# Optimization experiments

Measured on AMD Instinct MI355X. Metric: run time of the kernel, lower is better.

## Reference

```python
import jax, jax.numpy as jnp
import numpy as np

H = 16        # heads
DH = 64       # dim_head
DM = 1024     # query_dim = context_dim
INNER = H * DH


def setup_inputs() -> dict:
    key = jax.random.key(0)
    ks = jax.random.split(key, 5)
    s = 0.02
    queries = jax.random.normal(ks[0], (2, 2048, DM), dtype=jnp.float32)
    Wq = jax.random.normal(ks[1], (DM, INNER), dtype=jnp.float32) * s
    Wkv = jax.random.normal(ks[2], (DM, 2 * INNER), dtype=jnp.float32) * s
    Wo = jax.random.normal(ks[3], (INNER, DM), dtype=jnp.float32) * s
    bo = jax.random.normal(ks[4], (DM,), dtype=jnp.float32) * s
    return {"queries": queries, "Wq": Wq, "Wkv": Wkv, "Wo": Wo, "bo": bo}


def reference(queries, Wq, Wkv, Wo, bo):
    b, n, _ = queries.shape
    scale = DH ** -0.5
    q = queries @ Wq                       # [b, n, inner]
    kv = queries @ Wkv                     # self-attention: context = queries
    k, v = jnp.split(kv, 2, axis=-1)
    # b n (h d) -> b h n d
    split_heads = lambda t: t.reshape(b, n, H, DH).transpose(0, 2, 1, 3)
    q, k, v = map(split_heads, (q, k, v))
    sim = jnp.einsum('bhid,bhjd->bhij', q, k) * scale
    attn = jax.nn.softmax(sim, axis=-1)    # dropout is identity (p=0 / eval)
    out = jnp.einsum('bhij,bhjd->bhid', attn, v)
    out = out.transpose(0, 2, 1, 3).reshape(b, n, INNER)
    return out @ Wo + bo
```

## Files before the change

### kernel.cpp

```cpp
#include <hip/hip_runtime.h>
#include <math.h>
#include <stdint.h>

typedef _Float16 half8v __attribute__((ext_vector_type(8)));
typedef _Float16 half4v __attribute__((ext_vector_type(4)));
typedef float floatx4 __attribute__((ext_vector_type(4)));

#define MFMA16(a, b, c) __builtin_amdgcn_mfma_f32_16x16x32_f16(a, b, c, 0, 0, 0)

#define QSCALE 0.18033688011112f

__device__ __forceinline__ void gld_lds16(const void* g, void* l) {
  __builtin_amdgcn_global_load_lds(
      (const __attribute__((address_space(1))) uint32_t*)(uintptr_t)g,
      (__attribute__((address_space(3))) uint32_t*)(uintptr_t)l, 16, 0, 0);
}

__global__ __launch_bounds__(256) void convert_x(
    const float* __restrict__ X, _Float16* __restrict__ X16)
{
  size_t gid = (size_t)blockIdx.x * 256 + threadIdx.x;
  const float4* src = (const float4*)(X) + gid * 2;
  float4 a = src[0], b = src[1];
  half8v h;
  h[0]=(_Float16)a.x; h[1]=(_Float16)a.y; h[2]=(_Float16)a.z; h[3]=(_Float16)a.w;
  h[4]=(_Float16)b.x; h[5]=(_Float16)b.y; h[6]=(_Float16)b.z; h[7]=(_Float16)b.w;
  *((half8v*)X16 + gid) = h;
}

__global__ __launch_bounds__(256) void transpose_w(
    const float* __restrict__ Wq, const float* __restrict__ Wkv,
    const float* __restrict__ Wo,
    _Float16* __restrict__ WqkvT, _Float16* __restrict__ WoT)
{
  __shared__ alignas(16) _Float16 Tt[64 * 68];

  int b = blockIdx.x;
  const float* src; _Float16* dst; int N, tk, tn;
  if (b < 256)      { src = Wq;  dst = WqkvT;                 N = 1024; tk = b & 15;        tn = b >> 4; }
  else if (b < 768) { src = Wkv; dst = WqkvT + (size_t)1024 * 1024; N = 2048; tk = (b - 256) & 15; tn = (b - 256) >> 4; }
  else              { src = Wo;  dst = WoT;                   N = 1024; tk = (b - 768) & 15; tn = (b - 768) >> 4; }

  const int t = threadIdx.x;
  {
    int kg = t >> 4, ng = t & 15;
    const float* sp = src + (size_t)(tk * 64 + kg * 4) * N + tn * 64 + ng * 4;
    float4 r0 = *(const float4*)(sp);
    float4 r1 = *(const float4*)(sp + N);
    float4 r2 = *(const float4*)(sp + 2 * N);
    float4 r3 = *(const float4*)(sp + 3 * N);
    half4v h;
    h[0]=(_Float16)r0.x; h[1]=(_Float16)r1.x; h[2]=(_Float16)r2.x; h[3]=(_Float16)r3.x;
    *(half4v*)&Tt[(ng * 4 + 0) * 68 + kg * 4] = h;
    h[0]=(_Float16)r0.y; h[1]=(_Float16)r1.y; h[2]=(_Float16)r2.y; h[3]=(_Float16)r3.y;
    *(half4v*)&Tt[(ng * 4 + 1) * 68 + kg * 4] = h;
    h[0]=(_Float16)r0.z; h[1]=(_Float16)r1.z; h[2]=(_Float16)r2.z; h[3]=(_Float16)r3.z;
    *(half4v*)&Tt[(ng * 4 + 2) * 68 + kg * 4] = h;
    h[0]=(_Float16)r0.w; h[1]=(_Float16)r1.w; h[2]=(_Float16)r2.w; h[3]=(_Float16)r3.w;
    *(half4v*)&Tt[(ng * 4 + 3) * 68 + kg * 4] = h;
  }
  __syncthreads();
  #pragma unroll
  for (int i = 0; i < 2; i++) {
    int idx = t + i * 256;
    int nl = idx >> 3, k8 = (idx & 7) * 8;
    half8v v = *(half8v*)&Tt[nl * 68 + k8];
    *(half8v*)(dst + (size_t)(tn * 64 + nl) * 1024 + tk * 64 + k8) = v;
  }
}

__global__ __launch_bounds__(256) void qkv_gemm(
    const _Float16* __restrict__ X16, const _Float16* __restrict__ WqkvT,
    _Float16* __restrict__ q_ws, _Float16* __restrict__ k_ws,
    _Float16* __restrict__ vT_ws)
{
  constexpr int K = 1024;
  __shared__ alignas(16) _Float16 As[128 * 32];
  __shared__ alignas(16) _Float16 Bs[128 * 32];

  const int m0 = blockIdx.x * 128;
  const int n0 = blockIdx.y * 128;

  const int tid  = threadIdx.x;
  const int wave = tid >> 6, lane = tid & 63;
  const int qd = lane >> 4, l15 = lane & 15;
  const int wr = (wave >> 1) * 64, wc = (wave & 1) * 64;

  const int r0i = tid >> 2, c0 = (tid & 3) * 8;

  floatx4 acc[4][4] = {};

  for (int k0 = 0; k0 < K; k0 += 32) {
    gld_lds16(X16 + (size_t)(m0 + r0i) * K + k0 + c0, &As[tid * 8]);
    gld_lds16(X16 + (size_t)(m0 + 64 + r0i) * K + k0 + c0, &As[(tid + 256) * 8]);
    gld_lds16(WqkvT + (size_t)(n0 + r0i) * K + k0 + c0, &Bs[tid * 8]);
    gld_lds16(WqkvT + (size_t)(n0 + 64 + r0i) * K + k0 + c0, &Bs[(tid + 256) * 8]);
    __syncthreads();
    half8v a[4], b[4];
    #pragma unroll
    for (int it = 0; it < 4; it++)
      a[it] = *(half8v*)&As[(wr + it * 16 + l15) * 32 + qd * 8];
    #pragma unroll
    for (int jt = 0; jt < 4; jt++)
      b[jt] = *(half8v*)&Bs[(wc + jt * 16 + l15) * 32 + qd * 8];
    #pragma unroll
    for (int it = 0; it < 4; it++)
      #pragma unroll
      for (int jt = 0; jt < 4; jt++)
        acc[it][jt] = MFMA16(a[it], b[jt], acc[it][jt]);
    __syncthreads();
  }

  #pragma unroll
  for (int it = 0; it < 4; it++) {
    #pragma unroll
    for (int jt = 0; jt < 4; jt++) {
      #pragma unroll
      for (int r = 0; r < 4; r++) {
        int m = m0 + wr + it * 16 + qd * 4 + r;
        int n = n0 + wc + jt * 16 + l15;
        float val = acc[it][jt][r];
        int bb = m >> 11, nn = m & 2047;
        if (n0 < 1024) {
          int h = n >> 6, d = n & 63;
          q_ws[(((size_t)bb * 16 + h) * 2048 + nn) * 64 + d] = (_Float16)(val * QSCALE);
        } else if (n0 < 2048) {
          int c = n - 1024, h = c >> 6, d = c & 63;
          k_ws[(((size_t)bb * 16 + h) * 2048 + nn) * 64 + d] = (_Float16)val;
        } else {
          int c = n - 2048, h = c >> 6, d = c & 63;
          vT_ws[(((size_t)bb * 16 + h) * 64 + d) * 2048 + nn] = (_Float16)val;
        }
      }
    }
  }
}

__device__ __forceinline__ int swz(int row, int blk) {
  return row * 64 + ((blk ^ (row & 7)) << 3);
}

__global__ __launch_bounds__(128, 2) void attn_kernel(
    const _Float16* __restrict__ q_ws, const _Float16* __restrict__ k_ws,
    const _Float16* __restrict__ vT_ws, _Float16* __restrict__ aout)
{
  constexpr int N = 2048;
  __shared__ alignas(16) _Float16 Qs[64 * 64];
  __shared__ alignas(16) _Float16 Ks[64 * 64];
  __shared__ alignas(16) _Float16 Vts[64 * 64];

  const int qt = blockIdx.x;
  const int bh = blockIdx.y;
  const _Float16* Qp = q_ws + (size_t)bh * N * 64;
  const _Float16* Kp = k_ws + (size_t)bh * N * 64;
  const _Float16* Vp = vT_ws + (size_t)bh * 64 * N;

  const int tid = threadIdx.x, wave = tid >> 6, lane = tid & 63;
  const int qd = lane >> 4, l15 = lane & 15;
  const int q0 = qt * 64;
  const int wbase = wave * 32;

  #pragma unroll
  for (int i = 0; i < 4; i++) {
    int idx = tid + i * 128;
    int r = idx >> 3, blk = idx & 7;
    *(half8v*)&Qs[swz(r, blk)] =
        *(const half8v*)(Qp + (size_t)(q0 + r) * 64 + blk * 8);
  }
  __syncthreads();
  half8v qf[2][2];
  #pragma unroll
  for (int m = 0; m < 2; m++)
    #pragma unroll
    for (int ks = 0; ks < 2; ks++)
      qf[m][ks] = *(half8v*)&Qs[swz(wbase + m * 16 + l15, ks * 4 + qd)];

  floatx4 o[2][4] = {};
  float lsum[2][4] = {};

  half8v kpre[4], vpre[4];
  #pragma unroll
  for (int i = 0; i < 4; i++) {
    int idx = tid + i * 128;
    int r = idx >> 3, c8 = (idx & 7) * 8;
    kpre[i] = *(const half8v*)(Kp + (size_t)r * 64 + c8);
    vpre[i] = *(const half8v*)(Vp + (size_t)r * N + c8);
  }

  for (int kv0 = 0; kv0 < N; kv0 += 64) {
    __syncthreads();
    #pragma unroll
    for (int i = 0; i < 4; i++) {
      int idx = tid + i * 128;
      int r = idx >> 3, blk = idx & 7;
      *(half8v*)&Ks[swz(r, blk)]  = kpre[i];
      *(half8v*)&Vts[swz(r, blk)] = vpre[i];
    }
    if (kv0 + 64 < N) {
      int kvn = kv0 + 64;
      #pragma unroll
      for (int i = 0; i < 4; i++) {
        int idx = tid + i * 128;
        int r = idx >> 3, c8 = (idx & 7) * 8;
        kpre[i] = *(const half8v*)(Kp + (size_t)(kvn + r) * 64 + c8);
        vpre[i] = *(const half8v*)(Vp + (size_t)r * N + kvn + c8);
      }
    }
    __syncthreads();

    floatx4 s[2][4] = {};
    #pragma unroll
    for (int ks = 0; ks < 2; ks++) {
      half8v kf[4];
      #pragma unroll
      for (int nt = 0; nt < 4; nt++)
        kf[nt] = *(half8v*)&Ks[swz(nt * 16 + l15, ks * 4 + qd)];
      #pragma unroll
      for (int m = 0; m < 2; m++)
        #pragma unroll
        for (int nt = 0; nt < 4; nt++)
          s[m][nt] = MFMA16(qf[m][ks], kf[nt], s[m][nt]);
    }

    #pragma unroll
    for (int m = 0; m < 2; m++) {
      #pragma unroll
      for (int nt = 0; nt < 4; nt++) {
        #pragma unroll
        for (int r = 0; r < 4; r++) {
          float p = __builtin_amdgcn_exp2f(s[m][nt][r]);
          lsum[m][r] += p;
          int row = wbase + m * 16 + qd * 4 + r;
          int col = nt * 16 + l15;
          Qs[row * 64 + ((((col >> 3) ^ (row & 7)) << 3) | (col & 7))] =
              (_Float16)p;
        }
      }
    }

    #pragma unroll
    for (int ks = 0; ks < 2; ks++) {
      half8v pf[2], vf[4];
      #pragma unroll
      for (int m = 0; m < 2; m++)
        pf[m] = *(half8v*)&Qs[swz(wbase + m * 16 + l15, ks * 4 + qd)];
      #pragma unroll
      for (int nt = 0; nt < 4; nt++)
        vf[nt] = *(half8v*)&Vts[swz(nt * 16 + l15, ks * 4 + qd)];
      #pragma unroll
      for (int m = 0; m < 2; m++)
        #pragma unroll
        for (int nt = 0; nt < 4; nt++)
          o[m][nt] = MFMA16(pf[m], vf[nt], o[m][nt]);
    }
  }

  const int bb = bh >> 4, hh = bh & 15;
  #pragma unroll
  for (int m = 0; m < 2; m++) {
    #pragma unroll
    for (int r = 0; r < 4; r++) {
      float l = lsum[m][r];
      #pragma unroll
      for (int off = 1; off < 16; off <<= 1) l += __shfl_xor(l, off);
      float inv = 1.0f / l;
      int n = q0 + wbase + m * 16 + qd * 4 + r;
      #pragma unroll
      for (int nt = 0; nt < 4; nt++) {
        int d = nt * 16 + l15;
        aout[((size_t)(bb * 2048 + n)) * 1024 + hh * 64 + d] =
            (_Float16)(o[m][nt][r] * inv);
      }
    }
  }
}

__global__ __launch_bounds__(256) void out_gemm(
    const _Float16* __restrict__ A, const _Float16* __restrict__ WoT,
    const float* __restrict__ bo, float* __restrict__ Out)
{
  constexpr int K = 1024;
  __shared__ alignas(16) _Float16 As[128 * 32];
  __shared__ alignas(16) _Float16 Bs[128 * 32];

  const int m0 = blockIdx.x * 128;
  const int n0 = blockIdx.y * 128;
  const int tid = threadIdx.x;
  const int wave = tid >> 6, lane = tid & 63;
  const int qd = lane >> 4, l15 = lane & 15;
  const int wr = (wave >> 1) * 64, wc = (wave & 1) * 64;
  const int r0i = tid >> 2, c0 = (tid & 3) * 8;

  floatx4 acc[4][4] = {};

  for (int k0 = 0; k0 < K; k0 += 32) {
    gld_lds16(A + (size_t)(m0 + r0i) * K + k0 + c0, &As[tid * 8]);
    gld_lds16(A + (size_t)(m0 + 64 + r0i) * K + k0 + c0, &As[(tid + 256) * 8]);
    gld_lds16(WoT + (size_t)(n0 + r0i) * K + k0 + c0, &Bs[tid * 8]);
    gld_lds16(WoT + (size_t)(n0 + 64 + r0i) * K + k0 + c0, &Bs[(tid + 256) * 8]);
    __syncthreads();
    half8v a[4], b[4];
    #pragma unroll
    for (int it = 0; it < 4; it++)
      a[it] = *(half8v*)&As[(wr + it * 16 + l15) * 32 + qd * 8];
    #pragma unroll
    for (int jt = 0; jt < 4; jt++)
      b[jt] = *(half8v*)&Bs[(wc + jt * 16 + l15) * 32 + qd * 8];
    #pragma unroll
    for (int it = 0; it < 4; it++)
      #pragma unroll
      for (int jt = 0; jt < 4; jt++)
        acc[it][jt] = MFMA16(a[it], b[jt], acc[it][jt]);
    __syncthreads();
  }

  #pragma unroll
  for (int it = 0; it < 4; it++) {
    #pragma unroll
    for (int jt = 0; jt < 4; jt++) {
      int n = n0 + wc + jt * 16 + l15;
      float bias = bo[n];
      #pragma unroll
      for (int r = 0; r < 4; r++) {
        int m = m0 + wr + it * 16 + qd * 4 + r;
        Out[(size_t)m * 1024 + n] = acc[it][jt][r] + bias;
      }
    }
  }
}

extern "C" void kernel_launch(void* const* d_in, const int* in_sizes, int n_in,
                              void* d_out, int out_size, void* d_ws, size_t ws_size,
                              hipStream_t stream) {
  const float* X   = (const float*)d_in[0];
  const float* Wq  = (const float*)d_in[1];
  const float* Wkv = (const float*)d_in[2];
  const float* Wo  = (const float*)d_in[3];
  const float* bo  = (const float*)d_in[4];
  float* out = (float*)d_out;

  const size_t M4 = (size_t)4 * 1024 * 1024;
  _Float16* q_ws   = (_Float16*)d_ws;
  _Float16* k_ws   = q_ws + M4;
  _Float16* vT_ws  = k_ws + M4;
  _Float16* X16    = vT_ws + M4;
  _Float16* WqkvT  = X16 + M4;
  _Float16* WoT    = WqkvT + (size_t)3 * 1024 * 1024;
  _Float16* aout   = X16;

  convert_x<<<2048, 256, 0, stream>>>(X, X16);
  transpose_w<<<1024, 256, 0, stream>>>(Wq, Wkv, Wo, WqkvT, WoT);
  qkv_gemm<<<dim3(32, 24), 256, 0, stream>>>(X16, WqkvT, q_ws, k_ws, vT_ws);
  attn_kernel<<<dim3(32, 32), 128, 0, stream>>>(q_ws, k_ws, vT_ws, aout);
  out_gemm<<<dim3(32, 8), 256, 0, stream>>>(aout, WoT, bo, out);
}
```

Baseline: 198.1 us.

## Keep softmax probabilities in registers via transposed QK^T and remap attention grid

Computes S^T by swapping the MFMA operands (K as A, Q as B), so each lane's exp'd scores already match the A-operand layout of a 16x16x16 MFMA. P·V then runs directly from registers instead of writing P to LDS and reading it back. Row sums become per-lane partials reduced with two cross-quad shuffles at the end. The grid is also flattened and remapped so that 8 heads' blocks interleave, which changes the order K/V tiles are shared through L2. The cost is twice as many, half-width MFMAs for P·V and 8-byte LDS reads for V.

```diff
diff --git a/kernel.cpp b/kernel.cpp
--- a/kernel.cpp
+++ b/kernel.cpp
@@ -7,6 +7,7 @@
 typedef float floatx4 __attribute__((ext_vector_type(4)));
 
 #define MFMA16(a, b, c) __builtin_amdgcn_mfma_f32_16x16x32_f16(a, b, c, 0, 0, 0)
+#define MFMA16K16(a, b, c) __builtin_amdgcn_mfma_f32_16x16x16f16(a, b, c, 0, 0, 0)
 
 #define QSCALE 0.18033688011112f
 
@@ -85,7 +86,6 @@
   const int wave = tid >> 6, lane = tid & 63;
   const int qd = lane >> 4, l15 = lane & 15;
   const int wr = (wave >> 1) * 64, wc = (wave & 1) * 64;
-
   const int r0i = tid >> 2, c0 = (tid & 3) * 8;
 
   floatx4 acc[4][4] = {};
@@ -149,8 +149,10 @@
   __shared__ alignas(16) _Float16 Ks[64 * 64];
   __shared__ alignas(16) _Float16 Vts[64 * 64];
 
-  const int qt = blockIdx.x;
-  const int bh = blockIdx.y;
+  const int id = blockIdx.x;
+  const int bh = ((id >> 8) << 3) | (id & 7);
+  const int qt = (id >> 3) & 31;
+
   const _Float16* Qp = q_ws + (size_t)bh * N * 64;
   const _Float16* Kp = k_ws + (size_t)bh * N * 64;
   const _Float16* Vp = vT_ws + (size_t)bh * 64 * N;
@@ -176,7 +178,7 @@
       qf[m][ks] = *(half8v*)&Qs[swz(wbase + m * 16 + l15, ks * 4 + qd)];
 
   floatx4 o[2][4] = {};
-  float lsum[2][4] = {};
+  float lsum[2] = {};
 
   half8v kpre[4], vpre[4];
   #pragma unroll
@@ -208,7 +210,7 @@
     }
     __syncthreads();
 
-    floatx4 s[2][4] = {};
+    floatx4 s[4][2] = {};
     #pragma unroll
     for (int ks = 0; ks < 2; ks++) {
       half8v kf[4];
@@ -216,43 +218,47 @@
       for (int nt = 0; nt < 4; nt++)
         kf[nt] = *(half8v*)&Ks[swz(nt * 16 + l15, ks * 4 + qd)];
       #pragma unroll
-      for (int m = 0; m < 2; m++)
+      for (int nt = 0; nt < 4; nt++)
         #pragma unroll
-        for (int nt = 0; nt < 4; nt++)
-          s[m][nt] = MFMA16(qf[m][ks], kf[nt], s[m][nt]);
-    }
-
+        for (int m = 0; m < 2; m++)
+          s[nt][m] = MFMA16(kf[nt], qf[m][ks], s[nt][m]);
+    }
+
+    half4v pa[2][4];
     #pragma unroll
     for (int m = 0; m < 2; m++) {
       #pragma unroll
       for (int nt = 0; nt < 4; nt++) {
         #pragma unroll
         for (int r = 0; r < 4; r++) {
-          float p = __builtin_amdgcn_exp2f(s[m][nt][r]);
-          lsum[m][r] += p;
-          int row = wbase + m * 16 + qd * 4 + r;
-          int col = nt * 16 + l15;
-          Qs[row * 64 + ((((col >> 3) ^ (row & 7)) << 3) | (col & 7))] =
-              (_Float16)p;
+          float p = __builtin_amdgcn_exp2f(s[nt][m][r]);
+          lsum[m] += p;
+          pa[m][nt][r] = (_Float16)p;
         }
       }
     }
 
     #pragma unroll
-    for (int ks = 0; ks < 2; ks++) {
-      half8v pf[2], vf[4];
-      #pragma unroll
-      for (int m = 0; m < 2; m++)
-        pf[m] = *(half8v*)&Qs[swz(wbase + m * 16 + l15, ks * 4 + qd)];
-      #pragma unroll
-      for (int nt = 0; nt < 4; nt++)
-        vf[nt] = *(half8v*)&Vts[swz(nt * 16 + l15, ks * 4 + qd)];
+    for (int ks2 = 0; ks2 < 4; ks2++) {
+      half4v vf[4];
+      #pragma unroll
+      for (int dt = 0; dt < 4; dt++) {
+        int row = dt * 16 + l15;
+        int blk = 2 * ks2 + (qd >> 1);
+        vf[dt] = *(half4v*)&Vts[row * 64 + ((blk ^ (row & 7)) << 3) + (qd & 1) * 4];
+      }
       #pragma unroll
       for (int m = 0; m < 2; m++)
         #pragma unroll
-        for (int nt = 0; nt < 4; nt++)
-          o[m][nt] = MFMA16(pf[m], vf[nt], o[m][nt]);
-    }
+        for (int dt = 0; dt < 4; dt++)
+          o[m][dt] = MFMA16K16(pa[m][ks2], vf[dt], o[m][dt]);
+    }
+  }
+
+  #pragma unroll
+  for (int m = 0; m < 2; m++) {
+    lsum[m] += __shfl_xor(lsum[m], 16);
+    lsum[m] += __shfl_xor(lsum[m], 32);
   }
 
   const int bb = bh >> 4, hh = bh & 15;
@@ -260,16 +266,13 @@
   for (int m = 0; m < 2; m++) {
     #pragma unroll
     for (int r = 0; r < 4; r++) {
-      float l = lsum[m][r];
-      #pragma unroll
-      for (int off = 1; off < 16; off <<= 1) l += __shfl_xor(l, off);
-      float inv = 1.0f / l;
+      float inv = 1.0f / __shfl(lsum[m], qd * 4 + r);
       int n = q0 + wbase + m * 16 + qd * 4 + r;
       #pragma unroll
-      for (int nt = 0; nt < 4; nt++) {
-        int d = nt * 16 + l15;
+      for (int dt = 0; dt < 4; dt++) {
+        int d = dt * 16 + l15;
         aout[((size_t)(bb * 2048 + n)) * 1024 + hh * 64 + d] =
-            (_Float16)(o[m][nt][r] * inv);
+            (_Float16)(o[m][dt][r] * inv);
       }
     }
   }
@@ -351,6 +354,6 @@
   convert_x<<<2048, 256, 0, stream>>>(X, X16);
   transpose_w<<<1024, 256, 0, stream>>>(Wq, Wkv, Wo, WqkvT, WoT);
   qkv_gemm<<<dim3(32, 24), 256, 0, stream>>>(X16, WqkvT, q_ws, k_ws, vT_ws);
-  attn_kernel<<<dim3(32, 32), 128, 0, stream>>>(q_ws, k_ws, vT_ws, aout);
+  attn_kernel<<<1024, 128, 0, stream>>>(q_ws, k_ws, vT_ws, aout);
   out_gemm<<<dim3(32, 8), 256, 0, stream>>>(aout, WoT, bo, out);
 }
```

Result: no change. 196.8 us (-0.7%).
